# Kernel tuning notes

Measured on AMD Instinct MI355X. Metric: run time of the kernel, lower is better.

The kernel has to match this reference:

```python
import jax, jax.numpy as jnp
import numpy as np

N_PMTS = 12
N_TICKS = 550
BIN_SIGMA = 0.1
GAUSS_NORM = 1.0 / (BIN_SIGMA * 2.5066282746)
B, N_DEP, K = 8, 64, 512  # batch, depositions/event, electron slot cap per deposition


def setup_inputs() -> dict:
    key = jax.random.key(0)
    ks = jax.random.split(key, 10)
    # energy depositions [B, N, 4] = x, y, z, E(MeV)
    xy = jax.random.normal(ks[0], (B, N_DEP, 2), dtype=jnp.float32) * 5.0
    z = jax.random.uniform(ks[1], (B, N_DEP, 1), dtype=jnp.float32, minval=50.0, maxval=500.0)
    # E ~ 0.0115 MeV -> n = E*1e6/22.4 ~ up to ~513 electrons, capped at K
    E = jax.random.uniform(ks[2], (B, N_DEP, 1), dtype=jnp.float32, minval=0.002, maxval=0.0115)
    energy_depositions = jnp.concatenate([xy, z, E], axis=-1)
    return {
        "energy_depositions": energy_depositions,
        "e_draws": jax.random.normal(ks[3], (B, N_DEP), dtype=jnp.float32),
        "diff_draws": jax.random.normal(ks[4], (B, N_DEP, K, 3), dtype=jnp.float32),
        "unif_draws": jax.random.uniform(ks[5], (B, N_DEP, K), dtype=jnp.float32),
        "W1": jax.random.normal(ks[6], (2, 28), dtype=jnp.float32) * (1.0 / np.sqrt(2.0)),
        "b1": jnp.zeros((28,), dtype=jnp.float32),
        "W2": jax.random.normal(ks[7], (28, 12), dtype=jnp.float32) * (1.0 / np.sqrt(28.0)),
        "b2": jnp.zeros((12,), dtype=jnp.float32),
        "diffusion_scale": jnp.array([1.0, 1.0, 0.25], dtype=jnp.float32),
        "pmt_response_scale": jnp.ones((12,), dtype=jnp.float32),
        "lifetime": jnp.float32(25.0),
    }


def reference(energy_depositions, e_draws, diff_draws, unif_draws,
              W1, b1, W2, b2, diffusion_scale, pmt_response_scale, lifetime):
    dt = energy_depositions.dtype
    pos = energy_depositions[..., :3]            # [B,N,3]
    E = energy_depositions[..., 3]               # [B,N]
    # generate_electrons: n = E*1e6/22.4, sigma = sqrt(0.15 n)
    n = E * 1000.0 * 1000.0 / 22.4
    sigma = jnp.sqrt(0.15 * n)
    n_elec = jnp.clip((sigma * e_draws + n).astype(jnp.int32), 0, K)  # [B,N]
    slot_mask = jnp.arange(K)[None, None, :] < n_elec[..., None]       # [B,N,K]
    # diffuse_electrons: scale^2 * draw * sqrt(z) + position
    sqrt_z = jnp.sqrt(pos[..., 2])                                     # [B,N]
    elec = (diffusion_scale ** 2) * diff_draws * sqrt_z[..., None, None] + pos[:, :, None, :]  # [B,N,K,3]
    z_e = elec[..., 2]                                                 # [B,N,K]
    # apply_lifetime: accept with prob 1 - exp(-z/lifetime)
    prob = 1.0 - jnp.exp(-z_e / lifetime)
    mask = (slot_mask & (prob > unif_draws)).astype(dt)                # [B,N,K]
    # PMT response MLP on xy, scaled
    xy_e = elec[..., :2]
    h = jax.nn.sigmoid(xy_e @ W1 + b1)
    pmt = jax.nn.sigmoid(h @ W2 + b2) * (pmt_response_scale ** 2)      # [B,N,K,12]
    pmt = pmt * mask[..., None]
    # gaussian tick histogram over 550 ticks centered at 0.5..549.5
    ticks = jnp.arange(N_TICKS, dtype=dt) + 0.5
    g = GAUSS_NORM * jnp.exp(-((ticks - z_e[..., None]) ** 2) / BIN_SIGMA)  # [B,N,K,550]
    # sum over all electrons of the event: [B, 12, 550]
    return jnp.einsum('bnkp,bnkt->bpt', pmt, g)
```

## Files before the change

kernel.cpp:

```cpp
#include <hip/hip_runtime.h>
#include <hip/hip_fp16.h>

#define NB   8
#define NDEP 64
#define KK   512
#define NP   12
#define NT   550
#define BWIN 40
#define L2E  1.4426950408889634f


static __device__ __forceinline__ float fast_rcp(float x) {
    return __builtin_amdgcn_rcpf(x);
}
static __device__ __forceinline__ unsigned packh2(float a, float b) {
    __half2 h = __floats2half2_rn(a, b);
    return __builtin_bit_cast(unsigned, h);
}

__global__ __launch_bounds__(256) void init_kernel(
    const float* __restrict__ W1, const float* __restrict__ b1,
    const float* __restrict__ W2, const float* __restrict__ b2,
    const float* __restrict__ pscale,
    float* __restrict__ ws, float* __restrict__ out, int out_size)
{
    const int idx = blockIdx.x * 256 + threadIdx.x;
    for (int i = idx; i < out_size; i += gridDim.x * 256) out[i] = 0.0f;

    if (blockIdx.x == 0) {
        const int t = threadIdx.x;
        if (t < 28) {
            ws[t]      = W1[t]      * L2E;
            ws[28 + t] = W1[28 + t] * L2E;
            ws[56 + t] = b1[t]      * L2E;
        }
        if (t >= 64 && t < 232) {
            const int e = t - 64, j = e / 6, c = e - j * 6;
            ((unsigned*)(ws + 84))[e] = packh2(W2[j * NP + 2 * c], W2[j * NP + 2 * c + 1]);
        }
        if (t >= 232 && t < 238) {
            const int c = t - 232;
            ((unsigned*)(ws + 252))[c] = packh2(b2[2 * c], b2[2 * c + 1]);
        }
        if (t >= 238 && t < 250) {
            const int p = t - 238;
            ws[258 + p] = pscale[p] * pscale[p] * 3.9894228040143274f;
        }
    }
}

template<int S>
static __device__ __forceinline__ void gather_partial(
    const float* __restrict__ wl, int lane, int t_lo, int off,
    float* __restrict__ ppart)
{
    constexpr int W = 64 / S;
    const int tw  = lane & (W - 1);
    const int sub = lane / W;
    const float tc = (float)t_lo + (float)tw + 0.5f;

    float acc[NP];
    #pragma unroll
    for (int p = 0; p < NP; ++p) acc[p] = 0.0f;

    #pragma unroll 4
    for (int i = 0; i < W; ++i) {
        const int k = sub * W + i;
        const int o = (k << 4) + ((k >> 4) << 2);
        const float4 r0 = *(const float4*)&wl[o];
        const float4 r1 = *(const float4*)&wl[o + 4];
        const float4 r2 = *(const float4*)&wl[o + 8];
        const float ez  = wl[o + 12];
        const float d   = tc - ez;
        const float g   = exp2f(-14.426950408889634f * d * d);
        acc[0]  = fmaf(r0.x, g, acc[0]);  acc[1]  = fmaf(r0.y, g, acc[1]);
        acc[2]  = fmaf(r0.z, g, acc[2]);  acc[3]  = fmaf(r0.w, g, acc[3]);
        acc[4]  = fmaf(r1.x, g, acc[4]);  acc[5]  = fmaf(r1.y, g, acc[5]);
        acc[6]  = fmaf(r1.z, g, acc[6]);  acc[7]  = fmaf(r1.w, g, acc[7]);
        acc[8]  = fmaf(r2.x, g, acc[8]);  acc[9]  = fmaf(r2.y, g, acc[9]);
        acc[10] = fmaf(r2.z, g, acc[10]); acc[11] = fmaf(r2.w, g, acc[11]);
    }

    #pragma unroll
    for (int msk = W; msk < 64; msk <<= 1) {
        #pragma unroll
        for (int p = 0; p < NP; ++p) acc[p] += __shfl_xor(acc[p], msk);
    }

    if (lane < W) {
        float* pp = ppart + (size_t)(off + lane) * NP;
        *(float4*)&pp[0] = make_float4(acc[0], acc[1],  acc[2],  acc[3]);
        *(float4*)&pp[4] = make_float4(acc[4], acc[5],  acc[6],  acc[7]);
        *(float4*)&pp[8] = make_float4(acc[8], acc[9],  acc[10], acc[11]);
    }
}

__global__ __launch_bounds__(256) void next_sim_wave(
    const float* __restrict__ ed,
    const float* __restrict__ edraw,
    const float* __restrict__ ddraw,
    const float* __restrict__ udraw,
    const float* __restrict__ wst,
    const float* __restrict__ dscale, const float* __restrict__ life,
    float* __restrict__ out)
{
    __shared__ float rows[4][1040];
    __shared__ float part[4][BWIN * NP];
    __shared__ int2  hdr[4];

    const int tid  = threadIdx.x;
    const int lane = tid & 63;
    const int wid  = tid >> 6;
    const int bid  = blockIdx.x;
    const int bn   = bid >> 1;
    const int g    = ((bid & 1) << 2) | wid;
    const int b    = bn >> 6;

    const float4 dep = ((const float4*)ed)[bn];
    const float  edr = edraw[bn];
    const int    k   = (g << 6) + lane;
    const float* dd  = ddraw + ((size_t)bn * KK + k) * 3;
    const float d0 = dd[0], d1 = dd[1], d2 = dd[2];
    const float u  = udraw[(size_t)bn * KK + k];

    const float nval  = dep.w * (1000000.0f / 22.4f);
    const float sigma = sqrtf(0.15f * nval);
    int ne = (int)(sigma * edr + nval);
    ne = min(max(ne, 0), KK);
    const int tb = (int)floorf(dep.z) - BWIN / 2;
    const bool walive = ((g << 6) < ne);

    if (walive) {
        const float sqz     = sqrtf(dep.z);
        const float invLife = fast_rcp(life[0]);
        const float dS0 = dscale[0] * dscale[0];
        const float dS1 = dscale[1] * dscale[1];
        const float dS2 = dscale[2] * dscale[2];

        const float ez = fmaf(dS2 * d2, sqz, dep.z);
        const float ex = fmaf(dS0 * d0, sqz, dep.x);
        const float ey = fmaf(dS1 * d1, sqz, dep.y);
        const float prob = 1.0f - __expf(-ez * invLife);
        const float m = ((k < ne) && (prob > u)) ? 1.0f : 0.0f;

        const float*   w1a  = wst;
        const float*   w1b  = wst + 28;
        const float*   b1s  = wst + 56;
        const __half2* w2pk = (const __half2*)(wst + 84);
        const __half2* b2pk = (const __half2*)(wst + 252);
        const float*   qtab = wst + 258;

        __half2 pa0 = b2pk[0], pa1 = b2pk[1], pa2 = b2pk[2];
        __half2 pa3 = b2pk[3], pa4 = b2pk[4], pa5 = b2pk[5];
        #pragma unroll 4
        for (int j = 0; j < 28; ++j) {
            const float lg  = fmaf(w1a[j], ex, fmaf(w1b[j], ey, b1s[j]));
            const float hjf = fast_rcp(1.0f + exp2f(-lg));
            const __half2 h2 = __float2half2_rn(hjf);
            pa0 = __hfma2(h2, w2pk[j * 6 + 0], pa0);
            pa1 = __hfma2(h2, w2pk[j * 6 + 1], pa1);
            pa2 = __hfma2(h2, w2pk[j * 6 + 2], pa2);
            pa3 = __hfma2(h2, w2pk[j * 6 + 3], pa3);
            pa4 = __hfma2(h2, w2pk[j * 6 + 4], pa4);
            pa5 = __hfma2(h2, w2pk[j * 6 + 5], pa5);
        }
        float pm[NP];
        { float2 f;
          f = __half22float2(pa0); pm[0] = f.x; pm[1] = f.y;
          f = __half22float2(pa1); pm[2] = f.x; pm[3] = f.y;
          f = __half22float2(pa2); pm[4] = f.x; pm[5] = f.y;
          f = __half22float2(pa3); pm[6] = f.x; pm[7] = f.y;
          f = __half22float2(pa4); pm[8] = f.x; pm[9] = f.y;
          f = __half22float2(pa5); pm[10] = f.x; pm[11] = f.y; }

        float q[NP];
        #pragma unroll
        for (int p = 0; p < NP; ++p)
            q[p] = qtab[p] * m * fast_rcp(1.0f + exp2f(-pm[p] * L2E));

        float* wl = rows[wid];
        const int off = (lane << 4) + ((lane >> 4) << 2);
        *(float4*)&wl[off]     = make_float4(q[0], q[1],  q[2],  q[3]);
        *(float4*)&wl[off + 4] = make_float4(q[4], q[5],  q[6],  q[7]);
        *(float4*)&wl[off + 8] = make_float4(q[8], q[9],  q[10], q[11]);
        wl[off + 12] = ez;

        float ezmin = ez, ezmax = ez;
        #pragma unroll
        for (int msk = 1; msk < 64; msk <<= 1) {
            ezmin = fminf(ezmin, __shfl_xor(ezmin, msk));
            ezmax = fmaxf(ezmax, __shfl_xor(ezmax, msk));
        }
        const int fmin = (int)floorf(ezmin);
        const int fmax = (int)floorf(ezmax);
        const int need = fmax - fmin + 7;

        if (need <= 16) {
            const int t_lo = min(max(fmin - 3, tb), tb + BWIN - 16);
            gather_partial<4>(wl, lane, t_lo, t_lo - tb, part[wid]);
            if (lane == 0) hdr[wid] = make_int2(t_lo - tb, 16);
        } else {
            const int t_lo = min(max(fmin - 3, tb), tb + BWIN - 32);
            gather_partial<2>(wl, lane, t_lo, t_lo - tb, part[wid]);
            if (lane == 0) hdr[wid] = make_int2(t_lo - tb, 32);
        }
    } else {
        if (lane == 0) hdr[wid] = make_int2(0, 0);
    }
    __syncthreads();

    for (int idx = tid; idx < BWIN * NP; idx += 256) {
        const int t_rel = idx / NP;
        const int p     = idx - t_rel * NP;
        float s = 0.0f;
        #pragma unroll
        for (int w = 0; w < 4; ++w) {
            const int2 h  = hdr[w];
            const int  dt = t_rel - h.x;
            if ((unsigned)dt < (unsigned)h.y)
                s += part[w][t_rel * NP + p];
        }
        if (s != 0.0f)
            atomicAdd(&out[((size_t)b * NP + p) * NT + (tb + t_rel)], s);
    }
}

extern "C" void kernel_launch(void* const* d_in, const int* in_sizes, int n_in,
                              void* d_out, int out_size, void* d_ws, size_t ws_size,
                              hipStream_t stream) {
    const float* ed     = (const float*)d_in[0];
    const float* edraw  = (const float*)d_in[1];
    const float* ddraw  = (const float*)d_in[2];
    const float* udraw  = (const float*)d_in[3];
    const float* W1     = (const float*)d_in[4];
    const float* b1     = (const float*)d_in[5];
    const float* W2     = (const float*)d_in[6];
    const float* b2     = (const float*)d_in[7];
    const float* dscale = (const float*)d_in[8];
    const float* pscale = (const float*)d_in[9];
    const float* life   = (const float*)d_in[10];
    float* ws  = (float*)d_ws;
    float* out = (float*)d_out;

    init_kernel<<<64, 256, 0, stream>>>(W1, b1, W2, b2, pscale, ws, out, out_size);
    next_sim_wave<<<NB * NDEP * 2, 256, 0, stream>>>(
        ed, edraw, ddraw, udraw, ws, dscale, life, out);
}
```

Measured before the change: 20.91 us.

## Fuse init and simulation into one cooperative kernel with grid sync

Replaces the separate init and simulation launches with a single cooperative launch of 512 blocks. Each block first zeroes part of the output and block 0 packs the weights, then a grid-wide sync runs, and each block processes two virtual blocks of the simulation. This removes one kernel launch and the gap between kernels, at the cost of a grid barrier and half as many blocks, so each block does twice the work serially. If the cooperative launch fails, it falls back to the original two-kernel path.

```diff
diff --git a/kernel.cpp b/kernel.cpp
--- a/kernel.cpp
+++ b/kernel.cpp
@@ -1,5 +1,8 @@
 #include <hip/hip_runtime.h>
 #include <hip/hip_fp16.h>
+#include <hip/hip_cooperative_groups.h>
+
+namespace cg = cooperative_groups;
 
 #define NB   8
 #define NDEP 64
@@ -8,6 +11,8 @@
 #define NT   550
 #define BWIN 40
 #define L2E  1.4426950408889634f
+#define OUTN (NB * NP * NT)
+#define NBLK 512
 
 
 static __device__ __forceinline__ float fast_rcp(float x) {
@@ -18,34 +23,28 @@
     return __builtin_bit_cast(unsigned, h);
 }
 
-__global__ __launch_bounds__(256) void init_kernel(
+static __device__ __forceinline__ void pack_weights(
+    int tid,
     const float* __restrict__ W1, const float* __restrict__ b1,
     const float* __restrict__ W2, const float* __restrict__ b2,
-    const float* __restrict__ pscale,
-    float* __restrict__ ws, float* __restrict__ out, int out_size)
-{
-    const int idx = blockIdx.x * 256 + threadIdx.x;
-    for (int i = idx; i < out_size; i += gridDim.x * 256) out[i] = 0.0f;
-
-    if (blockIdx.x == 0) {
-        const int t = threadIdx.x;
-        if (t < 28) {
-            ws[t]      = W1[t]      * L2E;
-            ws[28 + t] = W1[28 + t] * L2E;
-            ws[56 + t] = b1[t]      * L2E;
-        }
-        if (t >= 64 && t < 232) {
-            const int e = t - 64, j = e / 6, c = e - j * 6;
-            ((unsigned*)(ws + 84))[e] = packh2(W2[j * NP + 2 * c], W2[j * NP + 2 * c + 1]);
-        }
-        if (t >= 232 && t < 238) {
-            const int c = t - 232;
-            ((unsigned*)(ws + 252))[c] = packh2(b2[2 * c], b2[2 * c + 1]);
-        }
-        if (t >= 238 && t < 250) {
-            const int p = t - 238;
-            ws[258 + p] = pscale[p] * pscale[p] * 3.9894228040143274f;
-        }
+    const float* __restrict__ pscale, float* __restrict__ wst)
+{
+    if (tid < 28) {
+        wst[tid]      = W1[tid]      * L2E;
+        wst[28 + tid] = W1[28 + tid] * L2E;
+        wst[56 + tid] = b1[tid]      * L2E;
+    }
+    if (tid >= 64 && tid < 232) {
+        const int e = tid - 64, j = e / 6, c = e - j * 6;
+        ((unsigned*)(wst + 84))[e] = packh2(W2[j * NP + 2 * c], W2[j * NP + 2 * c + 1]);
+    }
+    if (tid >= 232 && tid < 238) {
+        const int c = tid - 232;
+        ((unsigned*)(wst + 252))[c] = packh2(b2[2 * c], b2[2 * c + 1]);
+    }
+    if (tid >= 238 && tid < 250) {
+        const int p = tid - 238;
+        wst[258 + p] = pscale[p] * pscale[p] * 3.9894228040143274f;
     }
 }
 
@@ -95,25 +94,18 @@
     }
 }
 
-__global__ __launch_bounds__(256) void next_sim_wave(
-    const float* __restrict__ ed,
-    const float* __restrict__ edraw,
-    const float* __restrict__ ddraw,
-    const float* __restrict__ udraw,
-    const float* __restrict__ wst,
-    const float* __restrict__ dscale, const float* __restrict__ life,
-    float* __restrict__ out)
-{
-    __shared__ float rows[4][1040];
-    __shared__ float part[4][BWIN * NP];
-    __shared__ int2  hdr[4];
-
-    const int tid  = threadIdx.x;
+static __device__ __forceinline__ void sim_wave_body(
+    int vbid, int tid,
+    const float* __restrict__ ed,   const float* __restrict__ edraw,
+    const float* __restrict__ ddraw,const float* __restrict__ udraw,
+    const float* __restrict__ wst,  const float* __restrict__ dscale,
+    const float* __restrict__ life, float* __restrict__ out,
+    float (*rows)[1040], float (*part)[BWIN * NP], int2* hdr)
+{
     const int lane = tid & 63;
     const int wid  = tid >> 6;
-    const int bid  = blockIdx.x;
-    const int bn   = bid >> 1;
-    const int g    = ((bid & 1) << 2) | wid;
+    const int bn   = vbid >> 1;
+    const int g    = ((vbid & 1) << 2) | wid;
     const int b    = bn >> 6;
 
     const float4 dep = ((const float4*)ed)[bn];
@@ -225,6 +217,60 @@
     }
 }
 
+__global__ __launch_bounds__(256) void next_sim_coop(
+    const float* __restrict__ ed,   const float* __restrict__ edraw,
+    const float* __restrict__ ddraw,const float* __restrict__ udraw,
+    const float* __restrict__ W1, const float* __restrict__ b1,
+    const float* __restrict__ W2, const float* __restrict__ b2,
+    const float* __restrict__ dscale, const float* __restrict__ pscale,
+    const float* __restrict__ life,
+    float* __restrict__ wst, float* __restrict__ out)
+{
+    __shared__ float rows[4][1040];
+    __shared__ float part[4][BWIN * NP];
+    __shared__ int2  hdr[4];
+
+    const int tid = threadIdx.x;
+    const int bid = blockIdx.x;
+
+    {
+        const int zi = bid * 256 + tid;
+        if (zi < OUTN) out[zi] = 0.0f;
+        if (bid == 0) pack_weights(tid, W1, b1, W2, b2, pscale, wst);
+    }
+    cg::this_grid().sync();
+
+    sim_wave_body(bid, tid, ed, edraw, ddraw, udraw, wst, dscale, life, out,
+                  rows, part, hdr);
+    __syncthreads();
+    sim_wave_body(bid + NBLK, tid, ed, edraw, ddraw, udraw, wst, dscale, life, out,
+                  rows, part, hdr);
+}
+
+__global__ __launch_bounds__(256) void init_kernel(
+    const float* __restrict__ W1, const float* __restrict__ b1,
+    const float* __restrict__ W2, const float* __restrict__ b2,
+    const float* __restrict__ pscale,
+    float* __restrict__ ws, float* __restrict__ out, int out_size)
+{
+    const int idx = blockIdx.x * 256 + threadIdx.x;
+    for (int i = idx; i < out_size; i += gridDim.x * 256) out[i] = 0.0f;
+    if (blockIdx.x == 0) pack_weights(threadIdx.x, W1, b1, W2, b2, pscale, ws);
+}
+
+__global__ __launch_bounds__(256) void next_sim_wave(
+    const float* __restrict__ ed,   const float* __restrict__ edraw,
+    const float* __restrict__ ddraw,const float* __restrict__ udraw,
+    const float* __restrict__ wst,  const float* __restrict__ dscale,
+    const float* __restrict__ life, float* __restrict__ out)
+{
+    __shared__ float rows[4][1040];
+    __shared__ float part[4][BWIN * NP];
+    __shared__ int2  hdr[4];
+    sim_wave_body(blockIdx.x, threadIdx.x, ed, edraw, ddraw, udraw, wst,
+                  dscale, life, out, rows, part, hdr);
+}
+
 extern "C" void kernel_launch(void* const* d_in, const int* in_sizes, int n_in,
                               void* d_out, int out_size, void* d_ws, size_t ws_size,
                               hipStream_t stream) {
@@ -242,7 +288,18 @@
     float* ws  = (float*)d_ws;
     float* out = (float*)d_out;
 
-    init_kernel<<<64, 256, 0, stream>>>(W1, b1, W2, b2, pscale, ws, out, out_size);
-    next_sim_wave<<<NB * NDEP * 2, 256, 0, stream>>>(
-        ed, edraw, ddraw, udraw, ws, dscale, life, out);
-}
+    void* params[] = {
+        (void*)&ed, (void*)&edraw, (void*)&ddraw, (void*)&udraw,
+        (void*)&W1, (void*)&b1, (void*)&W2, (void*)&b2,
+        (void*)&dscale, (void*)&pscale, (void*)&life,
+        (void*)&ws, (void*)&out
+    };
+    hipError_t err = hipLaunchCooperativeKernel((const void*)next_sim_coop,
+                                                dim3(NBLK), dim3(256),
+                                                params, 0, stream);
+    if (err != hipSuccess) {
+        init_kernel<<<64, 256, 0, stream>>>(W1, b1, W2, b2, pscale, ws, out, out_size);
+        next_sim_wave<<<NB * NDEP * 2, 256, 0, stream>>>(
+            ed, edraw, ddraw, udraw, ws, dscale, life, out);
+    }
+}
```

Result: slower. 70.98 us (+239.5%).
